# Kernel optimization log

Hardware: AMD Instinct MI355X
Metric: run time of the kernel (lower is better)

Reference implementation:

```python
import jax, jax.numpy as jnp
import numpy as np

EPS = 1e-6      # vector-neurons EPS
BN_EPS = 1e-5   # torch BatchNorm2d default eps
NEG_SLOPE = 0.2 # VNLeakyReLU default
K = 20


def knn_idx(xf, k):
    # xf: (B, D, N) flattened features; returns (B, N, k) indices of nearest neighbors
    inner = -2.0 * jnp.einsum('bdn,bdm->bnm', xf, xf)
    xx = jnp.sum(xf * xf, axis=1)  # (B, N)
    neg_dist = -xx[:, :, None] - inner - xx[:, None, :]  # (B, N, N)
    _, idx = jax.lax.top_k(neg_dist, k)
    return idx


def get_graph_feature(x, k):
    # x: (B, C, 3, N) -> (B, 2C, 3, N, k)
    B, C, _, N = x.shape
    xf = x.reshape(B, C * 3, N)
    idx = knn_idx(xf, k)                      # (B, N, k)
    pts = x.transpose(0, 3, 1, 2)             # (B, N, C, 3)
    nbrs = jax.vmap(lambda p, i: p[i])(pts, idx)  # (B, N, k, C, 3)
    ctr = pts[:, :, None, :, :]               # (B, N, 1, C, 3)
    feat = jnp.concatenate([nbrs - ctr, jnp.broadcast_to(ctr, nbrs.shape)], axis=3)  # (B,N,k,2C,3)
    return feat.transpose(0, 3, 4, 1, 2)      # (B, 2C, 3, N, k)


def vn_batchnorm(p, gamma, beta):
    # p: (B, O, 3, N, K); BatchNorm2d on the vector norms (training-mode batch stats)
    norm = jnp.sqrt(jnp.sum(p * p, axis=2)) + EPS  # (B, O, N, K)
    mean = jnp.mean(norm, axis=(0, 2, 3))
    var = jnp.var(norm, axis=(0, 2, 3))            # biased, matches torch BN normalization
    g = gamma[None, :, None, None]
    b = beta[None, :, None, None]
    norm_bn = g * (norm - mean[None, :, None, None]) / jnp.sqrt(var[None, :, None, None] + BN_EPS) + b
    return p / norm[:, :, None] * norm_bn[:, :, None]


def vn_leaky_relu(p, Wd):
    d = jnp.einsum('oc,bcdnk->bodnk', Wd, p)
    dot = jnp.sum(p * d, axis=2, keepdims=True)
    d_nsq = jnp.sum(d * d, axis=2, keepdims=True)
    proj = p - (dot / (d_nsq + EPS)) * d
    return NEG_SLOPE * p + (1.0 - NEG_SLOPE) * jnp.where(dot >= 0, p, proj)


def setup_inputs() -> dict:
    key = jax.random.key(0)
    k1, k2, k3 = jax.random.split(key, 3)
    B, C, N = 2, 32, 8192
    out_feat, in_feat = 64, 64  # in_feat = 2*C
    x = jax.random.normal(k1, (B, C, 3, N), dtype=jnp.float32)
    W1 = jax.random.normal(k2, (out_feat, in_feat), dtype=jnp.float32) * (1.0 / np.sqrt(in_feat))
    Wd = jax.random.normal(k3, (out_feat, out_feat), dtype=jnp.float32) * (1.0 / np.sqrt(out_feat))
    gamma = jnp.ones((out_feat,), dtype=jnp.float32)
    beta = jnp.zeros((out_feat,), dtype=jnp.float32)
    return {"x": x, "W1": W1, "Wd": Wd, "gamma": gamma, "beta": beta}


def reference(x, W1, Wd, gamma, beta):
    # VNDGCNN.forward: get_graph_feature -> VNLinearAndLeakyReLU -> mean_pool over k
    feat = get_graph_feature(x, K)                       # (B, 2C, 3, N, k)
    p = jnp.einsum('oc,bcdnk->bodnk', W1, feat)          # VNLinear
    p = vn_batchnorm(p, gamma, beta)                     # VNBatchNorm (dim=5)
    p = vn_leaky_relu(p, Wd)                             # VNLeakyReLU
    return jnp.mean(p, axis=-1)                          # mean_pool -> (B, O, 3, N)
```

## Files before the change

kernel.cpp:

```cpp
#include <hip/hip_runtime.h>
#include <math.h>

#define NPTS 8192
#define NB 2
#define FDIM 96
#define KNN 20
#define VN_EPS 1e-6f
#define VN_BN_EPS 1e-5f
#define NSAMP 768
#define PSLOT 12
#define NPAN 64
#define ROWSLOT (NPAN * PSLOT)
#define CAPS 12
#define OVCAP 64

typedef float f32x16 __attribute__((ext_vector_type(16)));
typedef _Float16 f16x8 __attribute__((ext_vector_type(8)));
typedef unsigned short u16x8 __attribute__((ext_vector_type(8)));

#define WAVESYNC()                                            \
    do {                                                      \
        asm volatile("s_waitcnt lgkmcnt(0)" ::: "memory");    \
        __builtin_amdgcn_wave_barrier();                      \
        asm volatile("" ::: "memory");                        \
    } while (0)

__device__ __forceinline__ unsigned orderable(float v) {
    unsigned u = __float_as_uint(v);
    return (u & 0x80000000u) ? ~u : (u | 0x80000000u);
}
__device__ __forceinline__ float unorderable(unsigned k) {
    unsigned u = (k & 0x80000000u) ? (k & 0x7fffffffu) : ~k;
    return __uint_as_float(u);
}

__global__ __launch_bounds__(256) void k_prep(const float* __restrict__ x,
                                              float* __restrict__ xx,
                                              unsigned short* __restrict__ xs) {
    int m = blockIdx.x * 256 + threadIdx.x;
    int b = m >> 13, n = m & 8191;
    const float* xf = x + (size_t)b * FDIM * NPTS;
    unsigned short* row = xs + (size_t)m * 192;
    float s = 0.f;
    for (int fc = 0; fc < 12; ++fc) {
        u16x8 hv, lv;
        #pragma unroll
        for (int j = 0; j < 8; ++j) {
            float vv = xf[(size_t)(fc * 8 + j) * NPTS + n];
            s += vv * vv;
            _Float16 h = (_Float16)vv;
            float hf = (float)h;
            _Float16 l = (_Float16)(vv - hf);
            union { _Float16 f; unsigned short u; } ch, cl;
            ch.f = h; cl.f = l;
            hv[j] = ch.u; lv[j] = cl.u;
        }
        *(u16x8*)(row + fc * 8) = hv;
        *(u16x8*)(row + 96 + fc * 8) = lv;
    }
    xx[m] = s;
}


__global__ __launch_bounds__(256, 3) void k_thr(const unsigned short* __restrict__ xs,
                                                const float* __restrict__ xx,
                                                float* __restrict__ minibuf) {
    __shared__ __align__(16) unsigned short Bsl[128][104];
    __shared__ float sxr[128];
    __shared__ float sxc[128];
    int t = threadIdx.x;
    int lane = t & 63, wid = t >> 6;
    int l31 = lane & 31, hi = lane >> 5;
    int row0 = blockIdx.x * 128;
    int b = row0 >> 13;
    int panel = blockIdx.y;
    int m0 = panel * 128;
    const unsigned short* xsb = xs + (size_t)b * NPTS * 192;
    int n0w = (row0 & 8191) + wid * 32;

    f16x8 af[6];
    const unsigned short* arow = xsb + (size_t)(n0w + l31) * 192 + hi * 8;
    #pragma unroll
    for (int ks = 0; ks < 6; ++ks) af[ks] = *(const f16x8*)(arow + ks * 16);

    if (t < 128) {
        sxr[t] = xx[row0 + t];
        sxc[t] = xx[(b << 13) + m0 + t];
    }

    f32x16 acc[4];
    #pragma unroll
    for (int ct = 0; ct < 4; ++ct)
        #pragma unroll
        for (int e = 0; e < 16; ++e) acc[ct][e] = 0.f;

    int sc2 = t >> 1, sh2 = t & 1;
    auto stageB = [&](int part) {
        const unsigned short* sb = xsb + (size_t)(m0 + sc2) * 192 + part * 96 + sh2 * 48;
        unsigned short* db = &Bsl[sc2][sh2 * 48];
        #pragma unroll
        for (int j = 0; j < 6; ++j) *(u16x8*)(db + j * 8) = *(const u16x8*)(sb + j * 8);
    };
    auto mmpass = [&]() {
        #pragma unroll
        for (int ks = 0; ks < 6; ++ks)
            #pragma unroll
            for (int ct = 0; ct < 4; ++ct) {
                f16x8 bf = *(const f16x8*)&Bsl[ct * 32 + l31][ks * 16 + hi * 8];
                acc[ct] = __builtin_amdgcn_mfma_f32_32x32x16_f16(af[ks], bf, acc[ct], 0, 0, 0);
            }
    };

    stageB(1);
    __syncthreads();
    mmpass();
    __syncthreads();
    stageB(0);
    __syncthreads();
    mmpass();
    #pragma unroll
    for (int ks = 0; ks < 6; ++ks) af[ks] = *(const f16x8*)(arow + 96 + ks * 16);
    mmpass();

    float xc[4];
    #pragma unroll
    for (int ct = 0; ct < 4; ++ct) xc[ct] = sxc[ct * 32 + l31];
    #pragma unroll
    for (int q = 0; q < 4; ++q)
        #pragma unroll
        for (int rr = 0; rr < 4; ++rr) {
            int rowin = wid * 32 + 4 * hi + 8 * q + rr;
            float xr = sxr[rowin];
            #pragma unroll
            for (int ct = 0; ct < 4; ++ct) {
                float valx = 2.f * acc[ct][q * 4 + rr] - xr - xc[ct];
                minibuf[(size_t)(row0 + rowin) * NSAMP + m0 + ct * 32 + l31] = valx;
            }
        }
}

__global__ __launch_bounds__(256) void k_thrsel(const float* __restrict__ minibuf,
                                                float* __restrict__ tauF) {
    int t = threadIdx.x;
    int lane = t & 63, w = t >> 6;
    int r = blockIdx.x * 4 + w;
    const float* mp = minibuf + (size_t)r * NSAMP;
    unsigned key[12];
    #pragma unroll
    for (int s = 0; s < 12; ++s) key[s] = orderable(mp[lane + s * 64]);
    unsigned lo = 0, hi = 0x10000u;
    for (int it = 0; it < 16; ++it) {
        unsigned mid = (lo + hi) >> 1;
        unsigned mkey = mid << 16;
        int c = 0;
        #pragma unroll
        for (int s = 0; s < 12; ++s) c += (key[s] >= mkey) ? 1 : 0;
        #pragma unroll
        for (int d = 1; d < 64; d <<= 1) c += __shfl_xor(c, d);
        if (c >= KNN) lo = mid; else hi = mid;
    }
    if (lane == 0) tauF[r] = unorderable(lo << 16);
}

__global__ __launch_bounds__(256, 3) void k_distf(const unsigned short* __restrict__ xs,
                                                  const float* __restrict__ xx,
                                                  const float* __restrict__ tauF,
                                                  unsigned* __restrict__ cnt2d,
                                                  unsigned long long* __restrict__ cand,
                                                  unsigned* __restrict__ ovcnt,
                                                  unsigned long long* __restrict__ ovbuf) {
    __shared__ __align__(16) unsigned short Bsl[128][104];
    __shared__ float sxr[128];
    __shared__ float sxc[128];
    __shared__ float stau[128];
    int t = threadIdx.x;
    int lane = t & 63, wid = t >> 6;
    int l31 = lane & 31, hi = lane >> 5;
    int row0 = blockIdx.x * 128;
    int b = row0 >> 13;
    int panel = blockIdx.y;
    int m0 = panel * 128;
    const unsigned short* xsb = xs + (size_t)b * NPTS * 192;
    int n0w = (row0 & 8191) + wid * 32;

    f16x8 af[6];
    const unsigned short* arow = xsb + (size_t)(n0w + l31) * 192 + hi * 8;
    #pragma unroll
    for (int ks = 0; ks < 6; ++ks) af[ks] = *(const f16x8*)(arow + ks * 16);

    if (t < 128) {
        sxr[t] = xx[row0 + t];
        stau[t] = tauF[row0 + t];
        sxc[t] = xx[(b << 13) + m0 + t];
    }

    f32x16 acc[4];
    #pragma unroll
    for (int ct = 0; ct < 4; ++ct)
        #pragma unroll
        for (int e = 0; e < 16; ++e) acc[ct][e] = 0.f;

    int sc2 = t >> 1, sh2 = t & 1;
    auto stageB = [&](int part) {
        const unsigned short* sb = xsb + (size_t)(m0 + sc2) * 192 + part * 96 + sh2 * 48;
        unsigned short* db = &Bsl[sc2][sh2 * 48];
        #pragma unroll
        for (int j = 0; j < 6; ++j) *(u16x8*)(db + j * 8) = *(const u16x8*)(sb + j * 8);
    };
    auto mmpass = [&]() {
        #pragma unroll
        for (int ks = 0; ks < 6; ++ks)
            #pragma unroll
            for (int ct = 0; ct < 4; ++ct) {
                f16x8 bf = *(const f16x8*)&Bsl[ct * 32 + l31][ks * 16 + hi * 8];
                acc[ct] = __builtin_amdgcn_mfma_f32_32x32x16_f16(af[ks], bf, acc[ct], 0, 0, 0);
            }
    };

    stageB(1);
    __syncthreads();
    mmpass();
    __syncthreads();
    stageB(0);
    __syncthreads();
    mmpass();
    #pragma unroll
    for (int ks = 0; ks < 6; ++ks) af[ks] = *(const f16x8*)(arow + 96 + ks * 16);
    mmpass();

    float xc[4];
    #pragma unroll
    for (int ct = 0; ct < 4; ++ct) xc[ct] = sxc[ct * 32 + l31];
    #pragma unroll
    for (int q = 0; q < 4; ++q)
        #pragma unroll
        for (int rr = 0; rr < 4; ++rr) {
            int rowin = wid * 32 + 4 * hi + 8 * q + rr;
            int grow = row0 + rowin;
            float xr = sxr[rowin];
            float tau = stau[rowin];
            unsigned cnt_run = 0;
            size_t base = (size_t)grow * ROWSLOT + (size_t)panel * PSLOT;
            #pragma unroll
            for (int ct = 0; ct < 4; ++ct) {
                float valx = 2.f * acc[ct][q * 4 + rr] - xr - xc[ct];
                bool p = (valx >= tau);
                unsigned long long bal = __ballot(p);
                unsigned hm = hi ? (unsigned)(bal >> 32) : (unsigned)bal;
                if (p) {
                    unsigned key = orderable(valx);
                    unsigned pos = cnt_run + (unsigned)__popc(hm & ((1u << l31) - 1u));
                    unsigned long long e = ((unsigned long long)key << 32)
                                         | (unsigned)(m0 + ct * 32 + l31);
                    if (pos < PSLOT) {
                        cand[base + pos] = e;
                    } else {
                        unsigned o = atomicAdd(&ovcnt[grow], 1u);
                        if (o < OVCAP) ovbuf[(size_t)grow * OVCAP + o] = e;
                    }
                }
                cnt_run += (unsigned)__popc(hm);
            }
            if (l31 == 0)
                cnt2d[(size_t)grow * NPAN + panel] = (cnt_run < PSLOT) ? cnt_run : PSLOT;
        }
}

__global__ __launch_bounds__(256) void k_mrg(const unsigned long long* __restrict__ cand,
                                             const unsigned* __restrict__ cnt2d,
                                             const unsigned* __restrict__ ovcnt,
                                             const unsigned long long* __restrict__ ovbuf,
                                             int* __restrict__ idxOut) {
    int t = threadIdx.x;
    int lane = t & 63, w = t >> 6;
    int r = blockIdx.x * 4 + w;
    __shared__ unsigned scc[4][NPAN];
    scc[w][lane] = cnt2d[(size_t)r * NPAN + lane];
    WAVESYNC();
    const unsigned long long* cp = cand + (size_t)r * ROWSLOT;
    unsigned long long pk[CAPS + 1];
    #pragma unroll
    for (int s = 0; s < CAPS; ++s) {
        int slot = lane + 64 * s;
        int panel = slot / PSLOT;
        int within = slot - panel * PSLOT;
        pk[s] = (within < (int)scc[w][panel]) ? cp[slot] : 0ull;
    }
    int ovn = (int)ovcnt[r]; if (ovn > OVCAP) ovn = OVCAP;
    pk[CAPS] = (lane < ovn) ? ovbuf[(size_t)r * OVCAP + lane] : 0ull;

    unsigned lo = 0, hi = 0x10000u;
    for (int it = 0; it < 16; ++it) {
        unsigned mid = (lo + hi) >> 1;
        unsigned mkey = mid << 16;
        int c = 0;
        #pragma unroll
        for (int s = 0; s <= CAPS; ++s) c += ((unsigned)(pk[s] >> 32) >= mkey) ? 1 : 0;
        #pragma unroll
        for (int d = 1; d < 64; d <<= 1) c += __shfl_xor(c, d);
        if (c >= KNN) lo = mid; else hi = mid;
    }
    unsigned thr = lo << 16;

    __shared__ unsigned long long sk[4][128];
    __shared__ int sn[4];
    if (lane == 0) sn[w] = 0;
    WAVESYNC();
    #pragma unroll
    for (int s = 0; s <= CAPS; ++s) {
        if ((unsigned)(pk[s] >> 32) >= thr) {
            int j = atomicAdd(&sn[w], 1);
            if (j < 128) sk[w][j] = pk[s];
        }
    }
    WAVESYNC();
    int nc = sn[w]; if (nc > 128) nc = 128;
    #pragma unroll
    for (int half = 0; half < 2; ++half) {
        int i = lane + half * 64;
        if (i < nc) {
            unsigned long long me = sk[w][i];
            unsigned km = (unsigned)(me >> 32), cm = (unsigned)me;
            int rank = 0;
            for (int j = 0; j < nc; ++j) {
                unsigned long long o = sk[w][j];
                unsigned ko = (unsigned)(o >> 32), co = (unsigned)o;
                rank += (ko > km || (ko == km && co < cm)) ? 1 : 0;
            }
            if (rank < KNN) idxOut[(size_t)r * KNN + rank] = (int)cm;
        }
    }
}

__global__ __launch_bounds__(256) void k_uv(const float* __restrict__ x,
                                            const float* __restrict__ W1,
                                            float* __restrict__ u,
                                            float* __restrict__ v) {
    __shared__ float sA[64 * 33];
    __shared__ float sV[64 * 33];
    __shared__ float sxf[FDIM * 16];
    int t = threadIdx.x;
    for (int i = t; i < 64 * 32; i += 256) {
        int o = i >> 5, c = i & 31;
        float a = W1[o * 64 + c];
        sA[o * 33 + c] = a;
        sV[o * 33 + c] = W1[o * 64 + 32 + c] - a;
    }
    int p0 = blockIdx.x * 16;
    int b = p0 >> 13, nb = p0 & 8191;
    const float* xf = x + (size_t)b * FDIM * NPTS;
    for (int i = t; i < FDIM * 16; i += 256) {
        int f = i >> 4, p = i & 15;
        sxf[f * 16 + p] = xf[(size_t)f * NPTS + nb + p];
    }
    __syncthreads();
    #pragma unroll
    for (int ii = 0; ii < 4; ++ii) {
        int it = t + 256 * ii;
        int o = it & 63, p = it >> 6;
        float u0 = 0.f, u1 = 0.f, u2 = 0.f, w0 = 0.f, w1 = 0.f, w2 = 0.f;
        #pragma unroll
        for (int c = 0; c < 32; ++c) {
            float a = sA[o * 33 + c];
            float wv = sV[o * 33 + c];
            float x0 = sxf[(c * 3 + 0) * 16 + p];
            float x1 = sxf[(c * 3 + 1) * 16 + p];
            float x2 = sxf[(c * 3 + 2) * 16 + p];
            u0 += a * x0;  u1 += a * x1;  u2 += a * x2;
            w0 += wv * x0; w1 += wv * x1; w2 += wv * x2;
        }
        size_t base = ((size_t)(p0 + p) * 64 + o) * 3;
        u[base] = u0; u[base + 1] = u1; u[base + 2] = u2;
        v[base] = w0; v[base + 1] = w1; v[base + 2] = w2;
    }
}

__global__ __launch_bounds__(256) void k_stats(const float* __restrict__ u,
                                               const float* __restrict__ v,
                                               const int* __restrict__ idx,
                                               float* __restrict__ partial) {
    int blk = blockIdx.x, t = threadIdx.x;
    int o = t & 63, sub = t >> 6;
    int p0 = blk * 8;
    __shared__ float svf[8 * 192];
    __shared__ int sjf[8 * KNN];
    for (int i = t; i < 8 * 192; i += 256) svf[i] = v[(size_t)p0 * 192 + i];
    for (int i = t; i < 8 * KNN; i += 256) sjf[i] = idx[(size_t)p0 * KNN + i];
    __syncthreads();
    float s1 = 0.f, s2 = 0.f;
    for (int p = 0; p < 8; ++p) {
        int gpt = p0 + p;
        size_t ubase = (size_t)(gpt >> 13) * NPTS * 192;
        const float* vp = &svf[p * 192 + o * 3];
        float v0 = vp[0], v1 = vp[1], v2 = vp[2];
        for (int kk = sub; kk < KNN; kk += 4) {
            int j = sjf[p * KNN + kk];
            const float* up = u + ubase + (size_t)j * 192 + o * 3;
            float q0 = up[0] + v0, q1 = up[1] + v1, q2 = up[2] + v2;
            float nrm = sqrtf(q0 * q0 + q1 * q1 + q2 * q2) + VN_EPS;
            s1 += nrm;
            s2 += nrm * nrm;
        }
    }
    __shared__ float r1[256], r2[256];
    r1[t] = s1; r2[t] = s2;
    __syncthreads();
    if (t < 64) {
        float a1 = r1[t] + r1[t + 64] + r1[t + 128] + r1[t + 192];
        float a2 = r2[t] + r2[t + 64] + r2[t + 128] + r2[t + 192];
        partial[(size_t)blk * 128 + t] = a1;
        partial[(size_t)blk * 128 + 64 + t] = a2;
    }
}

__global__ __launch_bounds__(256) void k_reduce(const float* __restrict__ partial,
                                                const float* __restrict__ gamma,
                                                const float* __restrict__ beta,
                                                float* __restrict__ gsbs) {
    int ch = blockIdx.x, t = threadIdx.x;
    float s1 = 0.f, s2 = 0.f;
    for (int i = t; i < 2048; i += 256) {
        s1 += partial[(size_t)i * 128 + ch];
        s2 += partial[(size_t)i * 128 + 64 + ch];
    }
    __shared__ float r1[256], r2[256];
    r1[t] = s1; r2[t] = s2;
    __syncthreads();
    for (int s = 128; s > 0; s >>= 1) {
        if (t < s) { r1[t] += r1[t + s]; r2[t] += r2[t + s]; }
        __syncthreads();
    }
    if (t == 0) {
        const float cnt2 = (float)(NB * NPTS * KNN);
        float mean = r1[0] / cnt2;
        float var = r2[0] / cnt2 - mean * mean;
        float inv = 1.0f / sqrtf(var + VN_BN_EPS);
        float g = gamma[ch] * inv;
        gsbs[ch] = g;
        gsbs[64 + ch] = beta[ch] - mean * g;
    }
}

__global__ __launch_bounds__(64) void k_final(const float* __restrict__ u,
                                              const float* __restrict__ v,
                                              const int* __restrict__ idx,
                                              const float* __restrict__ Wd,
                                              const float* __restrict__ gsbs,
                                              float* __restrict__ out) {
    int lane = threadIdx.x;
    int l31 = lane & 31, hi = lane >> 5;
    int gpt = blockIdx.x;
    int b = gpt >> 13, n = gpt & 8191;

    __shared__ __align__(16) unsigned short Qw[30 * 72];
    __shared__ __align__(16) float Dw[30 * 64];

    f16x8 Bf[2][4];
    #pragma unroll
    for (int ct = 0; ct < 2; ++ct)
        #pragma unroll
        for (int ks = 0; ks < 4; ++ks) {
            const float* wp = Wd + (size_t)(ct * 32 + l31) * 64 + ks * 16 + hi * 8;
            f16x8 f;
            #pragma unroll
            for (int jj = 0; jj < 8; ++jj) f[jj] = (_Float16)wp[jj];
            Bf[ct][ks] = f;
        }

    float gso = gsbs[lane], bso = gsbs[64 + lane];
    size_t vb = (size_t)gpt * 192 + lane * 3;
    float v0 = v[vb], v1 = v[vb + 1], v2 = v[vb + 2];
    const int* jrow = idx + (size_t)gpt * KNN;
    size_t ubase = (size_t)b * NPTS * 192;
    float a0 = 0.f, a1 = 0.f, a2 = 0.f;

    for (int h = 0; h < 2; ++h) {
        #pragma unroll
        for (int kl = 0; kl < 10; ++kl) {
            int j = jrow[h * 10 + kl];
            const float* up = u + ubase + (size_t)j * 192 + lane * 3;
            float q0 = up[0] + v0, q1 = up[1] + v1, q2 = up[2] + v2;
            float nrm = sqrtf(q0 * q0 + q1 * q1 + q2 * q2) + VN_EPS;
            float f = (gso * nrm + bso) / nrm;
            q0 *= f; q1 *= f; q2 *= f;
            union { _Float16 f16; unsigned short u16; } c0, c1, c2;
            c0.f16 = (_Float16)q0; c1.f16 = (_Float16)q1; c2.f16 = (_Float16)q2;
            Qw[(3 * kl + 0) * 72 + lane] = c0.u16;
            Qw[(3 * kl + 1) * 72 + lane] = c1.u16;
            Qw[(3 * kl + 2) * 72 + lane] = c2.u16;
        }
        WAVESYNC();
        f32x16 acc[2];
        #pragma unroll
        for (int ct = 0; ct < 2; ++ct)
            #pragma unroll
            for (int e = 0; e < 16; ++e) acc[ct][e] = 0.f;
        #pragma unroll
        for (int ks = 0; ks < 4; ++ks) {
            f16x8 af = *(const f16x8*)&Qw[l31 * 72 + ks * 16 + hi * 8];
            acc[0] = __builtin_amdgcn_mfma_f32_32x32x16_f16(af, Bf[0][ks], acc[0], 0, 0, 0);
            acc[1] = __builtin_amdgcn_mfma_f32_32x32x16_f16(af, Bf[1][ks], acc[1], 0, 0, 0);
        }
        #pragma unroll
        for (int ct = 0; ct < 2; ++ct)
            #pragma unroll
            for (int q = 0; q < 4; ++q)
                #pragma unroll
                for (int r = 0; r < 4; ++r) {
                    int row = 4 * hi + 8 * q + r;
                    if (row < 30) Dw[row * 64 + ct * 32 + l31] = acc[ct][q * 4 + r];
                }
        WAVESYNC();
        #pragma unroll
        for (int kl = 0; kl < 10; ++kl) {
            float qd[3], dd[3];
            #pragma unroll
            for (int d = 0; d < 3; ++d) {
                union { unsigned short u16; _Float16 f16; } rr;
                rr.u16 = Qw[(3 * kl + d) * 72 + lane];
                qd[d] = (float)rr.f16;
                dd[d] = Dw[(3 * kl + d) * 64 + lane];
            }
            float dot = qd[0] * dd[0] + qd[1] * dd[1] + qd[2] * dd[2];
            float dn = dd[0] * dd[0] + dd[1] * dd[1] + dd[2] * dd[2];
            float coef = (dot >= 0.f) ? 0.f : 0.8f * dot / (dn + VN_EPS);
            a0 += qd[0] - coef * dd[0];
            a1 += qd[1] - coef * dd[1];
            a2 += qd[2] - coef * dd[2];
        }
        WAVESYNC();
    }
    float s = 1.f / (float)KNN;
    size_t ob = ((size_t)(b * 64 + lane) * 3) * NPTS + n;
    out[ob] = a0 * s;
    out[ob + NPTS] = a1 * s;
    out[ob + 2 * NPTS] = a2 * s;
}

extern "C" void kernel_launch(void* const* d_in, const int* in_sizes, int n_in,
                              void* d_out, int out_size, void* d_ws, size_t ws_size,
                              hipStream_t stream) {
    const float* x = (const float*)d_in[0];
    const float* W1 = (const float*)d_in[1];
    const float* Wd = (const float*)d_in[2];
    const float* gamma = (const float*)d_in[3];
    const float* beta = (const float*)d_in[4];
    float* out = (float*)d_out;

    char* ws = (char*)d_ws;
    size_t off = 0;
    auto alloc = [&](size_t bytes) {
        void* p = ws + off;
        off = (off + bytes + 255) & ~(size_t)255;
        return p;
    };
    const int totalRows = NB * NPTS;
    float* xxp = (float*)alloc((size_t)totalRows * 4);
    int* idxp = (int*)alloc((size_t)totalRows * KNN * 4);
    float* up = (float*)alloc((size_t)totalRows * 192 * 4);
    float* vp = (float*)alloc((size_t)totalRows * 192 * 4);
    float* partial = (float*)alloc((size_t)2048 * 128 * 4);
    float* gsbs = (float*)alloc(512);
    unsigned short* xsp = (unsigned short*)alloc((size_t)totalRows * 192 * 2);
    float* tauFp = (float*)alloc((size_t)totalRows * 4);
    unsigned* cnt2d = (unsigned*)alloc((size_t)totalRows * NPAN * 4);
    unsigned* ovcnt = (unsigned*)alloc((size_t)totalRows * 4);
    unsigned long long* ovbuf = (unsigned long long*)alloc((size_t)totalRows * OVCAP * 8);
    void* region = alloc((size_t)totalRows * ROWSLOT * 8);
    float* minibuf = (float*)region;
    unsigned long long* cand = (unsigned long long*)region;

    hipMemsetAsync(ovcnt, 0, (size_t)totalRows * 4, stream);

    k_prep<<<totalRows / 256, 256, 0, stream>>>(x, xxp, xsp);

    k_thr<<<dim3(totalRows / 128, NSAMP / 128), 256, 0, stream>>>(xsp, xxp, minibuf);
    k_thrsel<<<totalRows / 4, 256, 0, stream>>>(minibuf, tauFp);
    k_distf<<<dim3(totalRows / 128, NPAN), 256, 0, stream>>>(xsp, xxp, tauFp,
                                                             cnt2d, cand, ovcnt, ovbuf);
    k_mrg<<<totalRows / 4, 256, 0, stream>>>(cand, cnt2d, ovcnt, ovbuf, idxp);

    k_uv<<<totalRows / 16, 256, 0, stream>>>(x, W1, up, vp);
    k_stats<<<totalRows / 8, 256, 0, stream>>>(up, vp, idxp, partial);
    k_reduce<<<64, 256, 0, stream>>>(partial, gamma, beta, gsbs);
    k_final<<<totalRows, 64, 0, stream>>>(up, vp, idxp, Wd, gsbs, out);
}
```

Baseline: 390.7 us.

## Exploit distance symmetry by computing only upper-triangular tiles in kNN

The distance kernel now launches only upper-triangular 128x128 tiles per batch (2080 instead of 4096). Each off-diagonal tile also emits transposed candidates into the column points' candidate slots, with per-wave packed counts, and the merge kernel decodes those packed counts for lower panels. The goal is to roughly halve the MFMA distance work. In exchange it adds transposed scattered writes, a second ballot path and a sync per tile. The threshold is also loosened by one bucket so candidates that sit exactly on the boundary are kept.

```diff
diff --git a/kernel.cpp b/kernel.cpp
--- a/kernel.cpp
+++ b/kernel.cpp
@@ -13,6 +13,8 @@
 #define ROWSLOT (NPAN * PSLOT)
 #define CAPS 12
 #define OVCAP 64
+#define TSLOT 3
+#define NTILE 2080
 
 typedef float f32x16 __attribute__((ext_vector_type(16)));
 typedef _Float16 f16x8 __attribute__((ext_vector_type(8)));
@@ -60,7 +62,6 @@
     }
     xx[m] = s;
 }
-
 
 __global__ __launch_bounds__(256, 3) void k_thr(const unsigned short* __restrict__ xs,
                                                 const float* __restrict__ xx,
@@ -159,7 +160,9 @@
         for (int d = 1; d < 64; d <<= 1) c += __shfl_xor(c, d);
         if (c >= KNN) lo = mid; else hi = mid;
     }
-    if (lane == 0) tauF[r] = unorderable(lo << 16);
+    if (lane == 0) {
+        tauF[r] = (lo > 0u) ? unorderable((lo - 1u) << 16) : -3.4e38f;
+    }
 }
 
 __global__ __launch_bounds__(256, 3) void k_distf(const unsigned short* __restrict__ xs,
@@ -172,16 +175,26 @@
     __shared__ __align__(16) unsigned short Bsl[128][104];
     __shared__ float sxr[128];
     __shared__ float sxc[128];
-    __shared__ float stau[128];
+    __shared__ float stauR[128];
+    __shared__ float stauC[128];
+    __shared__ unsigned tcl[128][4];
     int t = threadIdx.x;
     int lane = t & 63, wid = t >> 6;
     int l31 = lane & 31, hi = lane >> 5;
-    int row0 = blockIdx.x * 128;
-    int b = row0 >> 13;
-    int panel = blockIdx.y;
-    int m0 = panel * 128;
-    const unsigned short* xsb = xs + (size_t)b * NPTS * 192;
-    int n0w = (row0 & 8191) + wid * 32;
+
+    int bx = blockIdx.x;
+    int batch = (bx >= NTILE) ? 1 : 0;
+    int ti = bx - batch * NTILE;
+    int R = 0;
+    while (ti >= 64 - R) { ti -= 64 - R; ++R; }
+    int C = R + ti;
+    bool offdiag = (R != C);
+    int rowL0 = R * 128;
+    int m0 = C * 128;
+    int rowG0 = batch * 8192 + rowL0;
+    int colG0 = batch * 8192 + m0;
+    const unsigned short* xsb = xs + (size_t)batch * NPTS * 192;
+    int n0w = rowL0 + wid * 32;
 
     f16x8 af[6];
     const unsigned short* arow = xsb + (size_t)(n0w + l31) * 192 + hi * 8;
@@ -189,9 +202,10 @@
     for (int ks = 0; ks < 6; ++ks) af[ks] = *(const f16x8*)(arow + ks * 16);
 
     if (t < 128) {
-        sxr[t] = xx[row0 + t];
-        stau[t] = tauF[row0 + t];
-        sxc[t] = xx[(b << 13) + m0 + t];
+        sxr[t] = xx[rowG0 + t];
+        stauR[t] = tauF[rowG0 + t];
+        sxc[t] = xx[colG0 + t];
+        stauC[t] = tauF[colG0 + t];
     }
 
     f32x16 acc[4];
@@ -228,19 +242,23 @@
     for (int ks = 0; ks < 6; ++ks) af[ks] = *(const f16x8*)(arow + 96 + ks * 16);
     mmpass();
 
-    float xc[4];
-    #pragma unroll
-    for (int ct = 0; ct < 4; ++ct) xc[ct] = sxc[ct * 32 + l31];
+    float xc[4], stC[4];
+    #pragma unroll
+    for (int ct = 0; ct < 4; ++ct) {
+        xc[ct] = sxc[ct * 32 + l31];
+        stC[ct] = stauC[ct * 32 + l31];
+    }
+    unsigned tq[4] = {0u, 0u, 0u, 0u};
     #pragma unroll
     for (int q = 0; q < 4; ++q)
         #pragma unroll
         for (int rr = 0; rr < 4; ++rr) {
             int rowin = wid * 32 + 4 * hi + 8 * q + rr;
-            int grow = row0 + rowin;
+            int grow = rowG0 + rowin;
             float xr = sxr[rowin];
-            float tau = stau[rowin];
+            float tau = stauR[rowin];
             unsigned cnt_run = 0;
-            size_t base = (size_t)grow * ROWSLOT + (size_t)panel * PSLOT;
+            size_t base = (size_t)grow * ROWSLOT + (size_t)C * PSLOT;
             #pragma unroll
             for (int ct = 0; ct < 4; ++ct) {
                 float valx = 2.f * acc[ct][q * 4 + rr] - xr - xc[ct];
@@ -260,10 +278,43 @@
                     }
                 }
                 cnt_run += (unsigned)__popc(hm);
+                if (offdiag) {
+                    bool pt = (valx >= stC[ct]);
+                    unsigned long long balT = __ballot(pt);
+                    unsigned b0 = (unsigned)((balT >> l31) & 1ull);
+                    unsigned b1 = (unsigned)((balT >> (l31 + 32)) & 1ull);
+                    if (pt) {
+                        unsigned pos = tq[ct] + (hi ? b0 : 0u);
+                        int cG = colG0 + ct * 32 + l31;
+                        unsigned keyt = orderable(valx);
+                        unsigned long long et = ((unsigned long long)keyt << 32)
+                                              | (unsigned)(rowL0 + rowin);
+                        if (pos < TSLOT) {
+                            cand[(size_t)cG * ROWSLOT + (size_t)R * PSLOT
+                                 + (size_t)wid * TSLOT + pos] = et;
+                        } else {
+                            unsigned o = atomicAdd(&ovcnt[cG], 1u);
+                            if (o < OVCAP) ovbuf[(size_t)cG * OVCAP + o] = et;
+                        }
+                    }
+                    tq[ct] += b0 + b1;
+                }
             }
             if (l31 == 0)
-                cnt2d[(size_t)grow * NPAN + panel] = (cnt_run < PSLOT) ? cnt_run : PSLOT;
-        }
+                cnt2d[(size_t)grow * NPAN + C] = (cnt_run < PSLOT) ? cnt_run : PSLOT;
+        }
+    if (offdiag) {
+        #pragma unroll
+        for (int ct = 0; ct < 4; ++ct) {
+            unsigned tv = tq[ct];
+            tcl[ct * 32 + l31][wid] = (tv < (unsigned)TSLOT) ? tv : (unsigned)TSLOT;
+        }
+        __syncthreads();
+        if (t < 128) {
+            unsigned pq = tcl[t][0] | (tcl[t][1] << 8) | (tcl[t][2] << 16) | (tcl[t][3] << 24);
+            cnt2d[(size_t)(colG0 + t) * NPAN + R] = pq;
+        }
+    }
 }
 
 __global__ __launch_bounds__(256) void k_mrg(const unsigned long long* __restrict__ cand,
@@ -274,6 +325,7 @@
     int t = threadIdx.x;
     int lane = t & 63, w = t >> 6;
     int r = blockIdx.x * 4 + w;
+    int B = (r & 8191) >> 7;
     __shared__ unsigned scc[4][NPAN];
     scc[w][lane] = cnt2d[(size_t)r * NPAN + lane];
     WAVESYNC();
@@ -284,7 +336,16 @@
         int slot = lane + 64 * s;
         int panel = slot / PSLOT;
         int within = slot - panel * PSLOT;
-        pk[s] = (within < (int)scc[w][panel]) ? cp[slot] : 0ull;
+        unsigned cc = scc[w][panel];
+        bool valid;
+        if (panel >= B) {
+            valid = within < (int)cc;
+        } else {
+            int wv = within / TSLOT;
+            int ws = within - wv * TSLOT;
+            valid = ws < (int)((cc >> (8 * wv)) & 255u);
+        }
+        pk[s] = valid ? cp[slot] : 0ull;
     }
     int ovn = (int)ovcnt[r]; if (ovn > OVCAP) ovn = OVCAP;
     pk[CAPS] = (lane < ovn) ? ovbuf[(size_t)r * OVCAP + lane] : 0ull;
@@ -576,8 +637,7 @@
 
     k_thr<<<dim3(totalRows / 128, NSAMP / 128), 256, 0, stream>>>(xsp, xxp, minibuf);
     k_thrsel<<<totalRows / 4, 256, 0, stream>>>(minibuf, tauFp);
-    k_distf<<<dim3(totalRows / 128, NPAN), 256, 0, stream>>>(xsp, xxp, tauFp,
-                                                             cnt2d, cand, ovcnt, ovbuf);
+    k_distf<<<NB * NTILE, 256, 0, stream>>>(xsp, xxp, tauFp, cnt2d, cand, ovcnt, ovbuf);
     k_mrg<<<totalRows / 4, 256, 0, stream>>>(cand, cnt2d, ovcnt, ovbuf, idxp);
 
     k_uv<<<totalRows / 16, 256, 0, stream>>>(x, W1, up, vp);
```

Result: no change. 386.2 us (-1.2%).
